# Performance work log

Hardware: AMD Instinct MI355X
Metric: run time of the kernel (lower is better)

## Reference

```python
import jax, jax.numpy as jnp
import numpy as np

IMG = 224      # img_size
P = 16         # patch_size
C = 3          # in_chans
K = 100        # n_segments
COMPACT = 10.0 # slic compactness
ITERS = 10     # slic k-means iterations


def _resize_matrix(src, dst):
    # Linear antialiased resize is a linear map; materialize it by resizing identity.
    return jax.image.resize(jnp.eye(src, dtype=jnp.float32), (dst, src),
                            method='linear', antialias=True)


def _slic_labels(img_hwc):
    """Simplified SLIC: grid-initialized k-means in (color, compactness-scaled xy) space."""
    H, W = IMG, IMG
    S = float(np.sqrt(H * W / K))         # superpixel spacing
    ratio = COMPACT / S                   # spatial scaling (SLIC distance weighting)
    yy, xx = jnp.meshgrid(jnp.arange(H, dtype=jnp.float32),
                          jnp.arange(W, dtype=jnp.float32), indexing='ij')
    feat = jnp.concatenate([img_hwc, (yy * ratio)[..., None], (xx * ratio)[..., None]],
                           axis=-1).reshape(H * W, C + 2)  # [HW, 5]
    # grid init of K centers
    gh = int(np.ceil(np.sqrt(K)))
    gw = int(np.ceil(K / gh))
    cy = ((np.arange(gh) + 0.5) * H / gh).astype(np.int32)
    cx = ((np.arange(gw) + 0.5) * W / gw).astype(np.int32)
    idx = (cy[:, None] * W + cx[None, :]).reshape(-1)[:K]
    centers0 = feat[jnp.asarray(idx)]  # [K, 5]

    f2 = jnp.sum(feat * feat, axis=1, keepdims=True)  # [HW,1]

    def dists(centers):
        c2 = jnp.sum(centers * centers, axis=1)  # [K]
        return f2 + c2[None, :] - 2.0 * (feat @ centers.T)  # [HW,K]

    def body(i, centers):
        lbl = jnp.argmin(dists(centers), axis=1)              # [HW]
        oh = jax.nn.one_hot(lbl, K, dtype=feat.dtype)         # [HW,K]
        cnt = oh.sum(0)                                       # [K]
        new = (oh.T @ feat) / jnp.maximum(cnt, 1.0)[:, None]  # [K,5]
        return jnp.where((cnt > 0)[:, None], new, centers)

    centers = jax.lax.fori_loop(0, ITERS, body, centers0)
    return jnp.argmin(dists(centers), axis=1).reshape(H, W)


def _embed_one(img_chw, A):
    img = jnp.transpose(img_chw, (1, 2, 0))                     # [H,W,C]
    labels = jax.lax.stop_gradient(_slic_labels(img))           # [H,W] int
    masks = jax.nn.one_hot(labels, K, dtype=img.dtype, axis=0)  # [K,H,W]
    masked = masks[..., None] * img[None]                       # [K,H,W,C]
    tmp = jnp.einsum('ph,khwc->kpwc', A, masked)                # resize rows
    return jnp.einsum('qw,kpwc->kpqc', A, tmp)                  # [K,P,P,C]


def reference(x):
    B = x.shape[0]
    A = _resize_matrix(IMG, P)
    sp = jax.vmap(lambda im: _embed_one(im, A))(x)  # [B,K,P,P,C]
    # torch: view(B, K*C, P, P)  (raw row-major reinterpret), flatten(2), transpose(1,2)
    out = sp.reshape(B, K * C, P, P).reshape(B, K * C, P * P)
    return jnp.transpose(out, (0, 2, 1))  # [B, P*P, K*C]


def setup_inputs() -> dict:
    key = jax.random.key(0)
    x = jax.random.uniform(key, (8, C, IMG, IMG), dtype=jnp.float32)
    return {"x": x}
```

## Files before the change

kernel.cpp:

```cpp
#include <hip/hip_runtime.h>
#include <math.h>

#define IMGD 224
#define HW 50176
#define NK 100
#define NB 8
#define OUT_PER_B 76800
#define NCHUNK 131
#define MSTR 13


static __device__ __forceinline__ float ratio_f32() {
  return (float)(10.0 / sqrt(224.0 * 224.0 / 100.0));
}

static __device__ __forceinline__ float dist5s(float f0, float f1, float f2,
                                               float f3, float f4, float fsq,
                                               float c0, float c1, float c2,
                                               float c3, float c4, float q) {
  float dot = __fmul_rn(f0, c0);
  dot = __fmaf_rn(f1, c1, dot);
  dot = __fmaf_rn(f2, c2, dot);
  dot = __fmaf_rn(f3, c3, dot);
  dot = __fmaf_rn(f4, c4, dot);
  return __fsub_rn(__fadd_rn(fsq, q), __fmul_rn(2.0f, dot));
}

static __device__ __forceinline__ float fsq5(float f0, float f1, float f2,
                                             float f3, float f4) {
  float s = __fmul_rn(f0, f0);
  s = __fadd_rn(s, __fmul_rn(f1, f1));
  s = __fadd_rn(s, __fmul_rn(f2, f2));
  s = __fadd_rn(s, __fmul_rn(f3, f3));
  s = __fadd_rn(s, __fmul_rn(f4, f4));
  return s;
}

__global__ void __launch_bounds__(128, 4) iter_kernel(
    const float* __restrict__ x, float* __restrict__ centers,
    const float* __restrict__ c2g, float* __restrict__ partials, int flag) {
  __shared__ float4 ck4[NK];
  __shared__ float2 ck2[NK];
  __shared__ unsigned int mask[NK * MSTR];
  __shared__ unsigned short ppk[NK * MSTR];
  __shared__ float4 cval4[384];
  __shared__ float  cvalf[384];
  __shared__ int cnt[128];
  __shared__ int offx[128];
  __shared__ int wtot;
  __shared__ float ubpart[12][10];
  __shared__ float ubg[12];
  __shared__ unsigned int candm[12][4];
  __shared__ unsigned char clist[12][104];
  __shared__ int clen[12];
  int c = blockIdx.x, b = blockIdx.y;
  int tid = threadIdx.x;
  int start = (c < 129) ? c * 384 : 49536 + (c - 129) * 320;
  int len   = (c < 129) ? 384 : 320;

  const float ratio = ratio_f32();
  const float* x0 = x + (size_t)b * 3 * HW;
  if (flag == 0) {
    if (tid < NK) {
      int gy = tid / 10, gx = tid - 10 * (tid / 10);
      int cy = (int)((gy + 0.5) * 224.0 / 10.0);
      int cx = (int)((gx + 0.5) * 224.0 / 10.0);
      int i = cy * IMGD + cx;
      float c0 = x0[i], c1 = x0[HW + i], c2 = x0[2 * HW + i];
      float c3 = __fmul_rn((float)cy, ratio);
      float c4 = __fmul_rn((float)cx, ratio);
      float s = __fmul_rn(c0, c0);
      s = __fadd_rn(s, __fmul_rn(c1, c1));
      s = __fadd_rn(s, __fmul_rn(c2, c2));
      s = __fadd_rn(s, __fmul_rn(c3, c3));
      s = __fadd_rn(s, __fmul_rn(c4, c4));
      ck4[tid] = make_float4(c0, c1, c2, c3);
      ck2[tid] = make_float2(c4, s);
      if (c == 0) {
        float* oc = centers + ((size_t)b * NK + tid) * 5;
        oc[0] = c0; oc[1] = c1; oc[2] = c2; oc[3] = c3; oc[4] = c4;
      }
    }
  } else {
    const float* cb = centers + (size_t)b * NK * 5;
    const float* c2b = c2g + (size_t)b * NK;
    if (tid < NK) {
      ck4[tid] = make_float4(cb[tid*5+0], cb[tid*5+1], cb[tid*5+2], cb[tid*5+3]);
      ck2[tid] = make_float2(cb[tid*5+4], c2b[tid]);
    }
  }
  for (int t = tid; t < NK * MSTR; t += 128) mask[t] = 0u;
  if (tid < 48) candm[tid >> 2][tid & 3] = 0u;

  float f0[3], f1[3], f2[3], f3[3], f4[3], fq[3];
  bool vld[3];
  for (int r = 0; r < 3; ++r) {
    int t = tid + r * 128;
    vld[r] = (t < len);
    int i = start + (vld[r] ? t : 0);
    int y = i / IMGD, xw = i - y * IMGD;
    f0[r] = x0[i]; f1[r] = x0[HW + i]; f2[r] = x0[2 * HW + i];
    f3[r] = __fmul_rn((float)y, ratio);
    f4[r] = __fmul_rn((float)xw, ratio);
    fq[r] = fsq5(f0[r], f1[r], f2[r], f3[r], f4[r]);
  }
  __syncthreads();

  if (tid < 120) {
    int g = tid / 10, kb = tid - 10 * g;
    int i0 = start + g * 32, i1 = i0 + 31;
    int ymin = i0 / IMGD, ymax = i1 / IMGD;
    int cmin = (ymin == ymax) ? (i0 - ymin * IMGD) : 0;
    int cmax = (ymin == ymax) ? (i1 - ymax * IMGD) : (IMGD - 1);
    float f3mn = __fmul_rn((float)ymin, ratio);
    float f3mx = __fmul_rn((float)ymax, ratio);
    float f4mn = __fmul_rn((float)cmin, ratio);
    float f4mx = __fmul_rn((float)cmax, ratio);
    float mn = 3.4e38f;
    for (int k = kb * 10; k < kb * 10 + 10; ++k) {
      float c3 = ck4[k].w, c4 = ck2[k].x;
      float dy = fmaxf(fabsf(c3 - f3mn), fabsf(c3 - f3mx));
      float dx = fmaxf(fabsf(c4 - f4mn), fabsf(c4 - f4mx));
      mn = fminf(mn, dy * dy + dx * dx + 3.0f);
    }
    ubpart[g][kb] = mn;
  }
  __syncthreads();
  if (tid < 12) {
    float mn = ubpart[tid][0];
    for (int j = 1; j < 10; ++j) mn = fminf(mn, ubpart[tid][j]);
    ubg[tid] = mn + 1.0f;
  }
  __syncthreads();
  if (tid < 120) {
    int g = tid / 10, kb = tid - 10 * g;
    int i0 = start + g * 32, i1 = i0 + 31;
    int ymin = i0 / IMGD, ymax = i1 / IMGD;
    int cmin = (ymin == ymax) ? (i0 - ymin * IMGD) : 0;
    int cmax = (ymin == ymax) ? (i1 - ymax * IMGD) : (IMGD - 1);
    float f3mn = __fmul_rn((float)ymin, ratio);
    float f3mx = __fmul_rn((float)ymax, ratio);
    float f4mn = __fmul_rn((float)cmin, ratio);
    float f4mx = __fmul_rn((float)cmax, ratio);
    float lim = ubg[g];
    for (int k = kb * 10; k < kb * 10 + 10; ++k) {
      float c3 = ck4[k].w, c4 = ck2[k].x;
      float dy = fmaxf(0.0f, fmaxf(f3mn - c3, c3 - f3mx));
      float dx = fmaxf(0.0f, fmaxf(f4mn - c4, c4 - f4mx));
      if (dy * dy + dx * dx <= lim)
        atomicOr(&candm[g][k >> 5], 1u << (k & 31));
    }
  }
  __syncthreads();
  if (tid < 12) {
    int len2 = 0;
    for (int w = 0; w < 4; ++w) {
      unsigned int m = candm[tid][w];
      while (m) {
        int j = __ffs(m) - 1;
        m &= m - 1;
        clist[tid][len2++] = (unsigned char)(w * 32 + j);
      }
    }
    clen[tid] = len2;
  }
  __syncthreads();

  float best[3]; int bk[3];
  for (int r = 0; r < 3; ++r) {
    best[r] = 3.4e38f; bk[r] = 0;
    int t = tid + r * 128;
    int g = (t < 384) ? (t >> 5) : 0;
    int n = clen[g];
    for (int j = 0; j < n; ++j) {
      int k = clist[g][j];
      float4 a4 = ck4[k];
      float2 a2 = ck2[k];
      float d = dist5s(f0[r], f1[r], f2[r], f3[r], f4[r], fq[r],
                       a4.x, a4.y, a4.z, a4.w, a2.x, a2.y);
      if (d < best[r]) { best[r] = d; bk[r] = k; }
    }
  }
  for (int r = 0; r < 3; ++r) {
    int t = tid + r * 128;
    if (vld[r]) atomicOr(&mask[bk[r] * MSTR + (t >> 5)], 1u << (t & 31));
  }
  __syncthreads();

  int myCnt = 0;
  if (tid < NK) {
    int s = 0;
    for (int g = 0; g < 12; ++g) {
      ppk[tid * MSTR + g] = (unsigned short)s;
      s += __popc(mask[tid * MSTR + g]);
    }
    myCnt = s;
  }
  cnt[tid] = myCnt;
  __syncthreads();

  int v = myCnt;
  for (int d = 1; d < 64; d <<= 1) {
    int u = __shfl_up(v, d, 64);
    if ((tid & 63) >= d) v += u;
  }
  if (tid == 63) wtot = v;
  __syncthreads();
  if (tid >= 64) v += wtot;
  offx[tid] = v;
  __syncthreads();

  for (int r = 0; r < 3; ++r) {
    int t = tid + r * 128;
    if (vld[r]) {
      int g = t >> 5, j = t & 31;
      unsigned int m = mask[bk[r] * MSTR + g];
      int rank = ppk[bk[r] * MSTR + g] + __popc(m & ((1u << j) - 1u));
      int pos = offx[bk[r]] - cnt[bk[r]] + rank;
      cval4[pos] = make_float4(f0[r], f1[r], f2[r], f3[r]);
      cvalf[pos] = f4[r];
    }
  }
  __syncthreads();

  if (tid < NK) {
    int n = cnt[tid];
    int base = offx[tid] - n;
    float s0 = 0.f, s1 = 0.f, s2 = 0.f, s3 = 0.f, s4 = 0.f, s5 = 0.f;
    for (int m = 0; m < n; ++m) {
      float4 vv = cval4[base + m];
      float ww = cvalf[base + m];
      s0 = __fadd_rn(s0, vv.x);
      s1 = __fadd_rn(s1, vv.y);
      s2 = __fadd_rn(s2, vv.z);
      s3 = __fadd_rn(s3, vv.w);
      s4 = __fadd_rn(s4, ww);
      s5 += 1.0f;
    }
    float* pp = partials + ((size_t)(b * NK + tid) * 6) * NCHUNK + c;
    pp[0 * NCHUNK] = s0; pp[1 * NCHUNK] = s1; pp[2 * NCHUNK] = s2;
    pp[3 * NCHUNK] = s3; pp[4 * NCHUNK] = s4; pp[5 * NCHUNK] = s5;
  }
}

__global__ void __launch_bounds__(128) combine_update_kernel(
    float* __restrict__ centers, const float* __restrict__ partials,
    float* __restrict__ c2g) {
  __shared__ float st[6 * NCHUNK];
  __shared__ float sums[6];
  __shared__ float newc[5];
  int bk = blockIdx.x;
  int tid = threadIdx.x;
  const float* base = partials + (size_t)bk * 6 * NCHUNK;
  for (int t = tid; t < 6 * NCHUNK; t += 128) st[t] = base[t];
  __syncthreads();
  if (tid < 6) {
    const float* row = st + tid * NCHUNK;
    float s = row[0];
    for (int c = 1; c < NCHUNK; ++c) s = __fadd_rn(s, row[c]);
    sums[tid] = s;
  }
  __syncthreads();
  float cntv = sums[5];
  float* cc = centers + (size_t)bk * 5;
  if (tid < 5) {
    float v;
    if (cntv > 0.0f) {
      float m = fmaxf(cntv, 1.0f);
      v = __fdiv_rn(sums[tid], m);
      cc[tid] = v;
    } else {
      v = cc[tid];
    }
    newc[tid] = v;
  }
  __syncthreads();
  if (tid == 0) {
    float t0 = __fmul_rn(newc[0], newc[0]);
    t0 = __fadd_rn(t0, __fmul_rn(newc[1], newc[1]));
    t0 = __fadd_rn(t0, __fmul_rn(newc[2], newc[2]));
    t0 = __fadd_rn(t0, __fmul_rn(newc[3], newc[3]));
    t0 = __fadd_rn(t0, __fmul_rn(newc[4], newc[4]));
    c2g[bk] = t0;
  }
}

__global__ void __launch_bounds__(256) embed_kernel(
    const float* __restrict__ x, const float* __restrict__ centers,
    const float* __restrict__ c2g, float* __restrict__ out) {
  __shared__ float red[256];
  __shared__ float Apv[28];
  __shared__ float Aqv[28];
  __shared__ float4 ck4[NK];
  __shared__ float2 ck2[NK];
  __shared__ float sk[NK * 3];
  __shared__ float ubk[128];
  __shared__ unsigned int candm[4];
  __shared__ unsigned char clist[NK];
  __shared__ int clen;
  int b = blockIdx.y;
  int p = blockIdx.x >> 4;
  int q = blockIdx.x & 15;
  int tid = threadIdx.x;

  float cp = (p + 0.5f) * 14.0f - 0.5f;
  float trip = 0.0f;
  if (tid < IMGD) {
    float xd = fabsf(cp - (float)tid) / 14.0f;
    trip = fmaxf(0.0f, 1.0f - xd);
  }
  red[tid] = trip;
  __syncthreads();
  for (int s = 128; s > 0; s >>= 1) {
    if (tid < s) red[tid] += red[tid + s];
    __syncthreads();
  }
  float Zp = red[0];
  __syncthreads();
  float cq = (q + 0.5f) * 14.0f - 0.5f;
  float triq = 0.0f;
  if (tid < IMGD) {
    float xd = fabsf(cq - (float)tid) / 14.0f;
    triq = fmaxf(0.0f, 1.0f - xd);
  }
  red[tid] = triq;
  __syncthreads();
  for (int s = 128; s > 0; s >>= 1) {
    if (tid < s) red[tid] += red[tid + s];
    __syncthreads();
  }
  float Zq = red[0];
  __syncthreads();

  int h0 = max(0, 14 * p - 7), h1 = min(IMGD - 1, 14 * p + 20);
  int w0 = max(0, 14 * q - 7), w1 = min(IMGD - 1, 14 * q + 20);
  int hl = h1 - h0 + 1, wl = w1 - w0 + 1;
  if (tid < hl) {
    float xd = fabsf(cp - (float)(h0 + tid)) / 14.0f;
    Apv[tid] = fmaxf(0.0f, 1.0f - xd) / Zp;
  }
  if (tid < wl) {
    float xd = fabsf(cq - (float)(w0 + tid)) / 14.0f;
    Aqv[tid] = fmaxf(0.0f, 1.0f - xd) / Zq;
  }
  const float* cb = centers + (size_t)b * NK * 5;
  const float* c2b = c2g + (size_t)b * NK;
  if (tid < NK) {
    ck4[tid] = make_float4(cb[tid*5+0], cb[tid*5+1], cb[tid*5+2], cb[tid*5+3]);
    ck2[tid] = make_float2(cb[tid*5+4], c2b[tid]);
  }
  for (int t = tid; t < NK * 3; t += 256) sk[t] = 0.0f;
  if (tid < 4) candm[tid] = 0u;
  __syncthreads();

  const float ratio = ratio_f32();
  float f3mn = __fmul_rn((float)h0, ratio);
  float f3mx = __fmul_rn((float)h1, ratio);
  float f4mn = __fmul_rn((float)w0, ratio);
  float f4mx = __fmul_rn((float)w1, ratio);
  if (tid < 128) {
    float u = 3.4e38f;
    if (tid < NK) {
      float c3 = ck4[tid].w, c4 = ck2[tid].x;
      float dy = fmaxf(fabsf(c3 - f3mn), fabsf(c3 - f3mx));
      float dx = fmaxf(fabsf(c4 - f4mn), fabsf(c4 - f4mx));
      u = dy * dy + dx * dx + 3.0f;
    }
    ubk[tid] = u;
  }
  __syncthreads();
  for (int s = 64; s > 0; s >>= 1) {
    if (tid < s) ubk[tid] = fminf(ubk[tid], ubk[tid + s]);
    __syncthreads();
  }
  float lim = ubk[0] + 1.0f;
  if (tid < NK) {
    float c3 = ck4[tid].w, c4 = ck2[tid].x;
    float dy = fmaxf(0.0f, fmaxf(f3mn - c3, c3 - f3mx));
    float dx = fmaxf(0.0f, fmaxf(f4mn - c4, c4 - f4mx));
    if (dy * dy + dx * dx <= lim)
      atomicOr(&candm[tid >> 5], 1u << (tid & 31));
  }
  __syncthreads();
  if (tid == 0) {
    int len2 = 0;
    for (int w = 0; w < 4; ++w) {
      unsigned int m = candm[w];
      while (m) {
        int j = __ffs(m) - 1;
        m &= m - 1;
        clist[len2++] = (unsigned char)(w * 32 + j);
      }
    }
    clen = len2;
  }
  __syncthreads();

  const float* xb = x + (size_t)b * 3 * HW;
  int n = hl * wl;
  int ncand = clen;
  for (int r = 0; r < 4; ++r) {
    int idx = tid + r * 256;
    if (idx >= n) break;
    int dh = idx / wl;
    int hh = h0 + dh;
    int dw = idx - dh * wl;
    int ww = w0 + dw;
    int i = hh * IMGD + ww;
    float v0 = xb[i], v1 = xb[HW + i], v2 = xb[2 * HW + i];
    float f3 = __fmul_rn((float)hh, ratio);
    float f4 = __fmul_rn((float)ww, ratio);
    float fq = fsq5(v0, v1, v2, f3, f4);
    float bestd = 3.4e38f; int bk = 0;
    for (int j = 0; j < ncand; ++j) {
      int k = clist[j];
      float4 a4 = ck4[k];
      float2 a2 = ck2[k];
      float d = dist5s(v0, v1, v2, f3, f4, fq,
                       a4.x, a4.y, a4.z, a4.w, a2.x, a2.y);
      if (d < bestd) { bestd = d; bk = k; }
    }
    float wgt = Apv[dh] * Aqv[dw];
    atomicAdd(&sk[bk * 3 + 0], wgt * v0);
    atomicAdd(&sk[bk * 3 + 1], wgt * v1);
    atomicAdd(&sk[bk * 3 + 2], wgt * v2);
  }
  __syncthreads();

  float* outb = out + (size_t)b * OUT_PER_B;
  int base = p * 48 + q * 3;
  for (int t = tid; t < NK * 3; t += 256) {
    int k = t / 3, c = t - 3 * k;
    int f = k * 768 + base + c;
    outb[(f & 255) * 300 + (f >> 8)] = sk[t];
  }
}

extern "C" void kernel_launch(void* const* d_in, const int* in_sizes, int n_in,
                              void* d_out, int out_size, void* d_ws, size_t ws_size,
                              hipStream_t stream) {
  const float* x = (const float*)d_in[0];
  float* out = (float*)d_out;
  char* ws = (char*)d_ws;
  float* centers  = (float*)(ws + 16384);
  float* c2g      = (float*)(ws + 49152);
  float* partials = (float*)(ws + 1703936);

  dim3 cgrid(NCHUNK, NB);
  iter_kernel<<<cgrid, 128, 0, stream>>>(x, centers, c2g, partials, 0);
  combine_update_kernel<<<NB * NK, 128, 0, stream>>>(centers, partials, c2g);
  for (int it = 1; it < 10; ++it) {
    iter_kernel<<<cgrid, 128, 0, stream>>>(x, centers, c2g, partials, 1);
    combine_update_kernel<<<NB * NK, 128, 0, stream>>>(centers, partials, c2g);
  }
  dim3 egrid(256, NB);
  embed_kernel<<<egrid, 256, 0, stream>>>(x, centers, c2g, out);
}
```

Baseline: 297.8 us.

## Compute final labels once per pixel and precompute resize weights in first iteration

Previously embed_kernel recomputed each pixel's argmin label inside every overlapping 28x28 window, so pixels were labeled up to four times, each time with a candidate pruning per window. A new label_kernel assigns each pixel once, with per-chunk candidate pruning, and writes byte labels. embed_kernel then only reads labels and accumulates. The antialiased resize weights are computed by extra blocks in the first iter_kernel launch, removing the per-block reductions from embed. This adds one kernel launch and a round trip of the labels through global memory.

```diff
diff --git a/kernel.cpp b/kernel.cpp
--- a/kernel.cpp
+++ b/kernel.cpp
@@ -38,7 +38,8 @@
 
 __global__ void __launch_bounds__(128, 4) iter_kernel(
     const float* __restrict__ x, float* __restrict__ centers,
-    const float* __restrict__ c2g, float* __restrict__ partials, int flag) {
+    const float* __restrict__ c2g, float* __restrict__ partials, int flag,
+    float* __restrict__ Ag) {
   __shared__ float4 ck4[NK];
   __shared__ float2 ck2[NK];
   __shared__ unsigned int mask[NK * MSTR];
@@ -53,8 +54,45 @@
   __shared__ unsigned int candm[12][4];
   __shared__ unsigned char clist[12][104];
   __shared__ int clen[12];
+  __shared__ float ared[128];
   int c = blockIdx.x, b = blockIdx.y;
   int tid = threadIdx.x;
+
+  if (c >= NCHUNK) {
+    for (int rr = 0; rr < 2; ++rr) {
+      int p = 2 * b + rr;
+      float cp = (p + 0.5f) * 14.0f - 0.5f;
+      float trip0, trip1 = 0.0f;
+      {
+        float xd = fabsf(cp - (float)tid) / 14.0f;
+        trip0 = fmaxf(0.0f, 1.0f - xd);
+      }
+      int t2 = tid + 128;
+      if (t2 < IMGD) {
+        float xd = fabsf(cp - (float)t2) / 14.0f;
+        trip1 = fmaxf(0.0f, 1.0f - xd);
+      }
+      ared[tid] = trip0 + trip1;
+      __syncthreads();
+      for (int s = 64; s > 0; s >>= 1) {
+        if (tid < s) ared[tid] += ared[tid + s];
+        __syncthreads();
+      }
+      float Zp = ared[0];
+      __syncthreads();
+      {
+        float xd = fabsf(cp - (float)tid) / 14.0f;
+        Ag[p * IMGD + tid] = fmaxf(0.0f, 1.0f - xd) / Zp;
+      }
+      if (t2 < IMGD) {
+        float xd = fabsf(cp - (float)t2) / 14.0f;
+        Ag[p * IMGD + t2] = fmaxf(0.0f, 1.0f - xd) / Zp;
+      }
+      __syncthreads();
+    }
+    return;
+  }
+
   int start = (c < 129) ? c * 384 : 49536 + (c - 129) * 320;
   int len   = (c < 129) ? 384 : 320;
 
@@ -285,120 +323,138 @@
   }
 }
 
-__global__ void __launch_bounds__(256) embed_kernel(
+__global__ void __launch_bounds__(128, 4) label_kernel(
     const float* __restrict__ x, const float* __restrict__ centers,
-    const float* __restrict__ c2g, float* __restrict__ out) {
-  __shared__ float red[256];
-  __shared__ float Apv[28];
-  __shared__ float Aqv[28];
+    const float* __restrict__ c2g, unsigned char* __restrict__ labels) {
   __shared__ float4 ck4[NK];
   __shared__ float2 ck2[NK];
-  __shared__ float sk[NK * 3];
-  __shared__ float ubk[128];
-  __shared__ unsigned int candm[4];
-  __shared__ unsigned char clist[NK];
-  __shared__ int clen;
-  int b = blockIdx.y;
-  int p = blockIdx.x >> 4;
-  int q = blockIdx.x & 15;
+  __shared__ float ubpart[12][10];
+  __shared__ float ubg[12];
+  __shared__ unsigned int candm[12][4];
+  int c = blockIdx.x, b = blockIdx.y;
   int tid = threadIdx.x;
-
-  float cp = (p + 0.5f) * 14.0f - 0.5f;
-  float trip = 0.0f;
-  if (tid < IMGD) {
-    float xd = fabsf(cp - (float)tid) / 14.0f;
-    trip = fmaxf(0.0f, 1.0f - xd);
-  }
-  red[tid] = trip;
-  __syncthreads();
-  for (int s = 128; s > 0; s >>= 1) {
-    if (tid < s) red[tid] += red[tid + s];
-    __syncthreads();
-  }
-  float Zp = red[0];
-  __syncthreads();
-  float cq = (q + 0.5f) * 14.0f - 0.5f;
-  float triq = 0.0f;
-  if (tid < IMGD) {
-    float xd = fabsf(cq - (float)tid) / 14.0f;
-    triq = fmaxf(0.0f, 1.0f - xd);
-  }
-  red[tid] = triq;
-  __syncthreads();
-  for (int s = 128; s > 0; s >>= 1) {
-    if (tid < s) red[tid] += red[tid + s];
-    __syncthreads();
-  }
-  float Zq = red[0];
-  __syncthreads();
-
-  int h0 = max(0, 14 * p - 7), h1 = min(IMGD - 1, 14 * p + 20);
-  int w0 = max(0, 14 * q - 7), w1 = min(IMGD - 1, 14 * q + 20);
-  int hl = h1 - h0 + 1, wl = w1 - w0 + 1;
-  if (tid < hl) {
-    float xd = fabsf(cp - (float)(h0 + tid)) / 14.0f;
-    Apv[tid] = fmaxf(0.0f, 1.0f - xd) / Zp;
-  }
-  if (tid < wl) {
-    float xd = fabsf(cq - (float)(w0 + tid)) / 14.0f;
-    Aqv[tid] = fmaxf(0.0f, 1.0f - xd) / Zq;
-  }
+  int start = (c < 129) ? c * 384 : 49536 + (c - 129) * 320;
+  int len   = (c < 129) ? 384 : 320;
+
+  const float ratio = ratio_f32();
+  const float* x0 = x + (size_t)b * 3 * HW;
   const float* cb = centers + (size_t)b * NK * 5;
   const float* c2b = c2g + (size_t)b * NK;
   if (tid < NK) {
     ck4[tid] = make_float4(cb[tid*5+0], cb[tid*5+1], cb[tid*5+2], cb[tid*5+3]);
     ck2[tid] = make_float2(cb[tid*5+4], c2b[tid]);
   }
-  for (int t = tid; t < NK * 3; t += 256) sk[t] = 0.0f;
-  if (tid < 4) candm[tid] = 0u;
-  __syncthreads();
-
-  const float ratio = ratio_f32();
-  float f3mn = __fmul_rn((float)h0, ratio);
-  float f3mx = __fmul_rn((float)h1, ratio);
-  float f4mn = __fmul_rn((float)w0, ratio);
-  float f4mx = __fmul_rn((float)w1, ratio);
-  if (tid < 128) {
-    float u = 3.4e38f;
-    if (tid < NK) {
-      float c3 = ck4[tid].w, c4 = ck2[tid].x;
+  if (tid < 48) candm[tid >> 2][tid & 3] = 0u;
+
+  float f0[3], f1[3], f2[3], f3[3], f4[3], fq[3];
+  int ii[3];
+  bool vld[3];
+  for (int r = 0; r < 3; ++r) {
+    int t = tid + r * 128;
+    vld[r] = (t < len);
+    int i = start + (vld[r] ? t : 0);
+    ii[r] = i;
+    int y = i / IMGD, xw = i - y * IMGD;
+    f0[r] = x0[i]; f1[r] = x0[HW + i]; f2[r] = x0[2 * HW + i];
+    f3[r] = __fmul_rn((float)y, ratio);
+    f4[r] = __fmul_rn((float)xw, ratio);
+    fq[r] = fsq5(f0[r], f1[r], f2[r], f3[r], f4[r]);
+  }
+  __syncthreads();
+
+  if (tid < 120) {
+    int g = tid / 10, kb = tid - 10 * g;
+    int i0 = start + g * 32, i1 = i0 + 31;
+    int ymin = i0 / IMGD, ymax = i1 / IMGD;
+    int cmin = (ymin == ymax) ? (i0 - ymin * IMGD) : 0;
+    int cmax = (ymin == ymax) ? (i1 - ymax * IMGD) : (IMGD - 1);
+    float f3mn = __fmul_rn((float)ymin, ratio);
+    float f3mx = __fmul_rn((float)ymax, ratio);
+    float f4mn = __fmul_rn((float)cmin, ratio);
+    float f4mx = __fmul_rn((float)cmax, ratio);
+    float mn = 3.4e38f;
+    for (int k = kb * 10; k < kb * 10 + 10; ++k) {
+      float c3 = ck4[k].w, c4 = ck2[k].x;
       float dy = fmaxf(fabsf(c3 - f3mn), fabsf(c3 - f3mx));
       float dx = fmaxf(fabsf(c4 - f4mn), fabsf(c4 - f4mx));
-      u = dy * dy + dx * dx + 3.0f;
-    }
-    ubk[tid] = u;
-  }
-  __syncthreads();
-  for (int s = 64; s > 0; s >>= 1) {
-    if (tid < s) ubk[tid] = fminf(ubk[tid], ubk[tid + s]);
-    __syncthreads();
-  }
-  float lim = ubk[0] + 1.0f;
-  if (tid < NK) {
-    float c3 = ck4[tid].w, c4 = ck2[tid].x;
-    float dy = fmaxf(0.0f, fmaxf(f3mn - c3, c3 - f3mx));
-    float dx = fmaxf(0.0f, fmaxf(f4mn - c4, c4 - f4mx));
-    if (dy * dy + dx * dx <= lim)
-      atomicOr(&candm[tid >> 5], 1u << (tid & 31));
-  }
-  __syncthreads();
-  if (tid == 0) {
-    int len2 = 0;
+      mn = fminf(mn, dy * dy + dx * dx + 3.0f);
+    }
+    ubpart[g][kb] = mn;
+  }
+  __syncthreads();
+  if (tid < 12) {
+    float mn = ubpart[tid][0];
+    for (int j = 1; j < 10; ++j) mn = fminf(mn, ubpart[tid][j]);
+    ubg[tid] = mn + 1.0f;
+  }
+  __syncthreads();
+  if (tid < 120) {
+    int g = tid / 10, kb = tid - 10 * g;
+    int i0 = start + g * 32, i1 = i0 + 31;
+    int ymin = i0 / IMGD, ymax = i1 / IMGD;
+    int cmin = (ymin == ymax) ? (i0 - ymin * IMGD) : 0;
+    int cmax = (ymin == ymax) ? (i1 - ymax * IMGD) : (IMGD - 1);
+    float f3mn = __fmul_rn((float)ymin, ratio);
+    float f3mx = __fmul_rn((float)ymax, ratio);
+    float f4mn = __fmul_rn((float)cmin, ratio);
+    float f4mx = __fmul_rn((float)cmax, ratio);
+    float lim = ubg[g];
+    for (int k = kb * 10; k < kb * 10 + 10; ++k) {
+      float c3 = ck4[k].w, c4 = ck2[k].x;
+      float dy = fmaxf(0.0f, fmaxf(f3mn - c3, c3 - f3mx));
+      float dx = fmaxf(0.0f, fmaxf(f4mn - c4, c4 - f4mx));
+      if (dy * dy + dx * dx <= lim)
+        atomicOr(&candm[g][k >> 5], 1u << (k & 31));
+    }
+  }
+  __syncthreads();
+
+  float best[3]; int bk[3];
+  for (int r = 0; r < 3; ++r) {
+    best[r] = 3.4e38f; bk[r] = 0;
+    int t = tid + r * 128;
+    int g = (t < 384) ? (t >> 5) : 0;
     for (int w = 0; w < 4; ++w) {
-      unsigned int m = candm[w];
+      unsigned int m = candm[g][w];
       while (m) {
         int j = __ffs(m) - 1;
         m &= m - 1;
-        clist[len2++] = (unsigned char)(w * 32 + j);
-      }
-    }
-    clen = len2;
-  }
+        int k = (w << 5) + j;
+        float4 a4 = ck4[k];
+        float2 a2 = ck2[k];
+        float d = dist5s(f0[r], f1[r], f2[r], f3[r], f4[r], fq[r],
+                         a4.x, a4.y, a4.z, a4.w, a2.x, a2.y);
+        if (d < best[r]) { best[r] = d; bk[r] = k; }
+      }
+    }
+  }
+  unsigned char* lb = labels + (size_t)b * HW;
+  for (int r = 0; r < 3; ++r)
+    if (vld[r]) lb[ii[r]] = (unsigned char)bk[r];
+}
+
+__global__ void __launch_bounds__(256) embed_kernel(
+    const float* __restrict__ x, const unsigned char* __restrict__ labels,
+    const float* __restrict__ Ag, float* __restrict__ out) {
+  __shared__ float Apv[28];
+  __shared__ float Aqv[28];
+  __shared__ float sk[NK * 3];
+  int b = blockIdx.y;
+  int p = blockIdx.x >> 4;
+  int q = blockIdx.x & 15;
+  int tid = threadIdx.x;
+
+  int h0 = max(0, 14 * p - 7), h1 = min(IMGD - 1, 14 * p + 20);
+  int w0 = max(0, 14 * q - 7), w1 = min(IMGD - 1, 14 * q + 20);
+  int hl = h1 - h0 + 1, wl = w1 - w0 + 1;
+  if (tid < hl) Apv[tid] = Ag[p * IMGD + h0 + tid];
+  if (tid < wl) Aqv[tid] = Ag[q * IMGD + w0 + tid];
+  for (int t = tid; t < NK * 3; t += 256) sk[t] = 0.0f;
   __syncthreads();
 
   const float* xb = x + (size_t)b * 3 * HW;
+  const unsigned char* lb = labels + (size_t)b * HW;
   int n = hl * wl;
-  int ncand = clen;
   for (int r = 0; r < 4; ++r) {
     int idx = tid + r * 256;
     if (idx >= n) break;
@@ -408,30 +464,19 @@
     int ww = w0 + dw;
     int i = hh * IMGD + ww;
     float v0 = xb[i], v1 = xb[HW + i], v2 = xb[2 * HW + i];
-    float f3 = __fmul_rn((float)hh, ratio);
-    float f4 = __fmul_rn((float)ww, ratio);
-    float fq = fsq5(v0, v1, v2, f3, f4);
-    float bestd = 3.4e38f; int bk = 0;
-    for (int j = 0; j < ncand; ++j) {
-      int k = clist[j];
-      float4 a4 = ck4[k];
-      float2 a2 = ck2[k];
-      float d = dist5s(v0, v1, v2, f3, f4, fq,
-                       a4.x, a4.y, a4.z, a4.w, a2.x, a2.y);
-      if (d < bestd) { bestd = d; bk = k; }
-    }
+    int k = lb[i];
     float wgt = Apv[dh] * Aqv[dw];
-    atomicAdd(&sk[bk * 3 + 0], wgt * v0);
-    atomicAdd(&sk[bk * 3 + 1], wgt * v1);
-    atomicAdd(&sk[bk * 3 + 2], wgt * v2);
+    atomicAdd(&sk[k * 3 + 0], wgt * v0);
+    atomicAdd(&sk[k * 3 + 1], wgt * v1);
+    atomicAdd(&sk[k * 3 + 2], wgt * v2);
   }
   __syncthreads();
 
   float* outb = out + (size_t)b * OUT_PER_B;
   int base = p * 48 + q * 3;
   for (int t = tid; t < NK * 3; t += 256) {
-    int k = t / 3, c = t - 3 * k;
-    int f = k * 768 + base + c;
+    int k = t / 3, cc = t - 3 * k;
+    int f = k * 768 + base + cc;
     outb[(f & 255) * 300 + (f >> 8)] = sk[t];
   }
 }
@@ -442,17 +487,21 @@
   const float* x = (const float*)d_in[0];
   float* out = (float*)d_out;
   char* ws = (char*)d_ws;
-  float* centers  = (float*)(ws + 16384);
-  float* c2g      = (float*)(ws + 49152);
-  float* partials = (float*)(ws + 1703936);
-
+  float* centers        = (float*)(ws + 16384);
+  float* c2g            = (float*)(ws + 49152);
+  float* Ag             = (float*)(ws + 65536);
+  unsigned char* labels = (unsigned char*)(ws + 98304);
+  float* partials       = (float*)(ws + 1703936);
+
+  dim3 cgrid0(NCHUNK + 1, NB);
   dim3 cgrid(NCHUNK, NB);
-  iter_kernel<<<cgrid, 128, 0, stream>>>(x, centers, c2g, partials, 0);
+  iter_kernel<<<cgrid0, 128, 0, stream>>>(x, centers, c2g, partials, 0, Ag);
   combine_update_kernel<<<NB * NK, 128, 0, stream>>>(centers, partials, c2g);
   for (int it = 1; it < 10; ++it) {
-    iter_kernel<<<cgrid, 128, 0, stream>>>(x, centers, c2g, partials, 1);
+    iter_kernel<<<cgrid, 128, 0, stream>>>(x, centers, c2g, partials, 1, Ag);
     combine_update_kernel<<<NB * NK, 128, 0, stream>>>(centers, partials, c2g);
   }
+  label_kernel<<<cgrid, 128, 0, stream>>>(x, centers, c2g, labels);
   dim3 egrid(256, NB);
-  embed_kernel<<<egrid, 256, 0, stream>>>(x, centers, c2g, out);
-}
+  embed_kernel<<<egrid, 256, 0, stream>>>(x, labels, Ag, out);
+}
```

New measurement: 294.9 us. Within noise of the previous version (-1.0%).
